# Optimization experiments

Hardware: AMD Instinct MI355X
Metric: run time of the kernel (lower is better)

The kernel has to match this reference:

```python
import jax, jax.numpy as jnp
import numpy as np

D_MODEL = 1024

def setup_inputs() -> dict:
    key = jax.random.key(0)
    k1, k2, k3, k4, k5 = jax.random.split(key, 5)
    B, T, C = 8, 4096, D_MODEL
    bound = 1.0 / np.sqrt(C)
    return {
        "x": jax.random.normal(k1, (B, T, C), dtype=jnp.float32),
        "W_state": jax.random.uniform(k2, (C, C), dtype=jnp.float32, minval=-bound, maxval=bound),
        "b_state": jax.random.uniform(k3, (C,), dtype=jnp.float32, minval=-bound, maxval=bound),
        "W_gate": jax.random.uniform(k4, (C, C), dtype=jnp.float32, minval=-bound, maxval=bound),
        "b_gate": jax.random.uniform(k5, (C,), dtype=jnp.float32, minval=-bound, maxval=bound),
    }

def reference(x, W_state, b_state, W_gate, b_gate):
    # x: [B, T, C]. Precompute both projections as large batched GEMMs
    # (input-dependent parts have no time dependency), then scan the
    # tanh recurrence + sigmoid gating over T.
    B, T, C = x.shape
    px = jnp.einsum('btc,dc->btd', x, W_state) + b_state          # [B,T,C]
    g = jax.nn.sigmoid(jnp.einsum('btc,dc->btd', x, W_gate) + b_gate)  # [B,T,C]

    def step(state, inp):
        p_t, g_t = inp                    # each [B, C]
        state = jnp.tanh(p_t + state)
        return state, g_t * state

    s0 = jnp.zeros((B, C), dtype=x.dtype)
    final_state, outs = jax.lax.scan(
        step, s0, (px.transpose(1, 0, 2), g.transpose(1, 0, 2)))
    return outs.transpose(1, 0, 2), final_state  # [B,T,C], [B,C]
```

## Files before the change

kernel.cpp:

```cpp
#include <hip/hip_runtime.h>

#define DB 8
#define DT 4096
#define DC 1024
#define GM (DB*DT)
#define GN (2*DC)
#define GK DC

#define SEG 128
#define NSEG (DT/SEG)
#define WU 64
#define UCH 16

typedef _Float16 f16;
typedef _Float16 f16x8 __attribute__((ext_vector_type(8)));
typedef _Float16 f16x4 __attribute__((ext_vector_type(4)));
typedef float    f32x4 __attribute__((ext_vector_type(4)));

__device__ __forceinline__ void async_copy16(const void* g, void* l) {
    __builtin_amdgcn_global_load_lds((const __attribute__((address_space(1))) void*)g,
                                     (__attribute__((address_space(3))) void*)l,
                                     16, 0, 0);
}

__global__ __launch_bounds__(256) void conv_x_kernel(const float* __restrict__ x,
                                                     f16* __restrict__ xh) {
    const size_t i = (size_t)blockIdx.x * 256 + threadIdx.x;
    const f32x4 v = *(const f32x4*)(x + 4*i);
    f16x4 h; h.x = (f16)v.x; h.y = (f16)v.y; h.z = (f16)v.z; h.w = (f16)v.w;
    *(f16x4*)(xh + 4*i) = h;
}

__global__ __launch_bounds__(256) void conv_w_kernel(const float* __restrict__ Ws,
                                                     const float* __restrict__ Wg,
                                                     f16* __restrict__ wc) {
    const int i = blockIdx.x * 256 + threadIdx.x;
    const int e = i * 4;
    const int n = e >> 10;
    const int k = e & 1023;
    const float* src = (n < DC) ? (Ws + (size_t)n * DC + k)
                                : (Wg + (size_t)(n - DC) * DC + k);
    const f32x4 v = *(const f32x4*)src;
    f16x4 h; h.x = (f16)v.x; h.y = (f16)v.y; h.z = (f16)v.z; h.w = (f16)v.w;
    *(f16x4*)(wc + e) = h;
}

template<bool GF16>
__global__ __launch_bounds__(256, 2) void gemm_kernel(
        const f16* __restrict__ xh, const f16* __restrict__ wc,
        const float* __restrict__ b_state, const float* __restrict__ b_gate,
        f16* __restrict__ pxh, f16* __restrict__ gh, float* __restrict__ outg) {
    __shared__ f16 lds_a[128 * 64];
    __shared__ f16 lds_b[128 * 64];

    const int tid  = threadIdx.x;
    const int lane = tid & 63;
    const int bn   = blockIdx.x & 15;
    const int bm   = blockIdx.x >> 4;
    const int wave = tid >> 6;
    const int wm   = (wave & 1) * 64;
    const int wn   = (wave >> 1) * 64;
    const int lr   = lane & 15;
    const int lq   = lane >> 4;

    f32x4 acc[4][4] = {};

    const int kc = tid & 7;
    const int rw = tid >> 3;
    const int ldsbase = (tid & 192) * 16;

    for (int kt = 0; kt < GK / 64; ++kt) {
        const int k0 = kt * 64;
        #pragma unroll
        for (int i = 0; i < 4; ++i) {
            const int row = i * 32 + rw;
            async_copy16(xh + (size_t)(bm * 128 + row) * GK + k0 + kc * 8,
                         (char*)lds_a + ldsbase + i * 4096);
            async_copy16(wc + (size_t)(bn * 128 + row) * GK + k0 + kc * 8,
                         (char*)lds_b + ldsbase + i * 4096);
        }
        __syncthreads();
        #pragma unroll
        for (int ks = 0; ks < 2; ++ks) {
            f16x8 af[4], bf[4];
            #pragma unroll
            for (int t = 0; t < 4; ++t) {
                af[t] = *(const f16x8*)&lds_a[(wm + t * 16 + lr) * 64 + ks * 32 + lq * 8];
                bf[t] = *(const f16x8*)&lds_b[(wn + t * 16 + lr) * 64 + ks * 32 + lq * 8];
            }
            #pragma unroll
            for (int im = 0; im < 4; ++im)
                #pragma unroll
                for (int in = 0; in < 4; ++in)
                    acc[im][in] = __builtin_amdgcn_mfma_f32_16x16x32_f16(
                        af[im], bf[in], acc[im][in], 0, 0, 0);
        }
        __syncthreads();
    }

    const int gm0 = bm * 128 + wm + lq * 4;
    const int gn0 = bn * 128 + wn + lr;
    if (bn < 8) {
        #pragma unroll
        for (int in = 0; in < 4; ++in) {
            const int gn = gn0 + in * 16;
            const float bias = b_state[gn];
            #pragma unroll
            for (int im = 0; im < 4; ++im) {
                const int gm = gm0 + im * 16;
                #pragma unroll
                for (int r = 0; r < 4; ++r)
                    pxh[(size_t)(gm + r) * DC + gn] = (f16)(acc[im][in][r] + bias);
            }
        }
    } else {
        #pragma unroll
        for (int in = 0; in < 4; ++in) {
            const int gn   = gn0 + in * 16;
            const int gcol = gn - DC;
            const float bias = b_gate[gcol];
            #pragma unroll
            for (int im = 0; im < 4; ++im) {
                const int gm = gm0 + im * 16;
                #pragma unroll
                for (int r = 0; r < 4; ++r) {
                    const float v = acc[im][in][r] + bias;
                    const float sg = 1.0f / (1.0f + __expf(-v));
                    if (GF16) gh[(size_t)(gm + r) * DC + gcol] = (f16)sg;
                    else      outg[(size_t)(gm + r) * DC + gcol] = sg;
                }
            }
        }
    }
}

template<bool GF16>
__global__ __launch_bounds__(256, 4) void scan_kernel(
        const f16* __restrict__ ph, const f16* __restrict__ gh,
        float* __restrict__ out) {
    const int tau   = blockIdx.x * 256 + threadIdx.x;
    const int seg   = tau >> 13;
    const int chain = tau & 8191;
    const size_t base = (size_t)(chain >> 10) * ((size_t)DT * DC) + (chain & 1023);
    const float L = 2.8853900817779268f;
    float sL = 0.0f, s = 0.0f;
    const int t0 = seg * SEG;

    if (seg) {
        const int tw = t0 - WU;
        f16 wA[UCH], wB[UCH];
        #pragma unroll
        for (int i = 0; i < UCH; ++i) wA[i] = ph[base + (size_t)(tw + i) * DC];
        #pragma unroll 1
        for (int ch = 0; ch < WU / UCH; ++ch) {
            #pragma unroll
            for (int i = 0; i < UCH; ++i)
                wB[i] = ph[base + (size_t)(tw + (ch + 1) * UCH + i) * DC];
            #pragma unroll
            for (int i = 0; i < UCH; ++i) {
                const float u = fmaf((float)wA[i], L, sL);
                const float e = __builtin_amdgcn_exp2f(u);
                const float r = __builtin_amdgcn_rcpf(e + 1.0f);
                sL = fmaf(-2.0f * L, r, L);
            }
            #pragma unroll
            for (int i = 0; i < UCH; ++i) wA[i] = wB[i];
        }
    }

    float pA[UCH], pB[UCH], gA[UCH], gB[UCH];
    #pragma unroll
    for (int i = 0; i < UCH; ++i) {
        const size_t idx = base + (size_t)(t0 + i) * DC;
        pA[i] = (float)ph[idx] * L;
        gA[i] = GF16 ? (float)gh[idx] : out[idx];
    }
    #pragma unroll 1
    for (int ch = 0; ch < SEG / UCH; ++ch) {
        if (GF16 || (ch + 1 < SEG / UCH)) {
            #pragma unroll
            for (int i = 0; i < UCH; ++i) {
                const size_t idx = base + (size_t)(t0 + (ch + 1) * UCH + i) * DC;
                pB[i] = (float)ph[idx] * L;
                gB[i] = GF16 ? (float)gh[idx] : out[idx];
            }
        }
        #pragma unroll
        for (int i = 0; i < UCH; ++i) {
            const float u = pA[i] + sL;
            const float e = __builtin_amdgcn_exp2f(u);
            const float r = __builtin_amdgcn_rcpf(e + 1.0f);
            s  = fmaf(-2.0f, r, 1.0f);
            sL = fmaf(-2.0f * L, r, L);
            out[base + (size_t)(t0 + ch * UCH + i) * DC] = gA[i] * s;
        }
        #pragma unroll
        for (int i = 0; i < UCH; ++i) { pA[i] = pB[i]; gA[i] = gB[i]; }
    }
    if (seg == NSEG - 1) out[(size_t)DB * DT * DC + chain] = s;
}

extern "C" void kernel_launch(void* const* d_in, const int* in_sizes, int n_in,
                              void* d_out, int out_size, void* d_ws, size_t ws_size,
                              hipStream_t stream) {
    const float* x  = (const float*)d_in[0];
    const float* Ws = (const float*)d_in[1];
    const float* bs = (const float*)d_in[2];
    const float* Wg = (const float*)d_in[3];
    const float* bg = (const float*)d_in[4];
    float* out = (float*)d_out;

    char* ws = (char*)d_ws;
    const size_t SZ_XH  = (size_t)GM * GK * 2;
    const size_t SZ_WC  = (size_t)GN * GK * 2;
    const size_t SZ_PXH = ((size_t)GM + UCH) * DC * 2;
    const size_t NEED_F16 = SZ_XH + SZ_WC + 2 * SZ_PXH;

    f16* xh = (f16*)ws;
    f16* wc = (f16*)(ws + SZ_XH);
    f16* pxh = (f16*)(ws + SZ_XH + SZ_WC);
    const bool gf16 = (ws_size >= NEED_F16);
    f16* gh = gf16 ? (f16*)(ws + SZ_XH + SZ_WC + SZ_PXH) : (f16*)nullptr;

    conv_x_kernel<<<dim3(GM * GK / 1024), dim3(256), 0, stream>>>(x, xh);
    conv_w_kernel<<<dim3(GN * GK / 1024), dim3(256), 0, stream>>>(Ws, Wg, wc);
    if (gf16) {
        gemm_kernel<true><<<dim3(4096), dim3(256), 0, stream>>>(
            xh, wc, bs, bg, pxh, gh, out);
        scan_kernel<true><<<dim3(1024), dim3(256), 0, stream>>>(pxh, gh, out);
    } else {
        gemm_kernel<false><<<dim3(4096), dim3(256), 0, stream>>>(
            xh, wc, bs, bg, pxh, gh, out);
        scan_kernel<false><<<dim3(1024), dim3(256), 0, stream>>>(pxh, gh, out);
    }
}
```

Baseline: 451.7 us.

## Swizzle GEMM LDS, remap blocks per XCD, shorten scan segments, drop fp32 gate path

The GEMM tile loads now use an XOR swizzle on the k-chunk index, so the MFMA fragment reads from LDS avoid bank conflicts. Block indices are remapped so each XCD works on a contiguous band of M rows, which should improve L2 reuse of the A tiles, and the occupancy hint rises to 4 blocks per CU. The scan segments are halved to 64 steps (with an 8-step chunk), doubling the parallel chains while keeping the same 64-step warm-up, so redundant warm-up work per output grows. The fallback that stored the fp32 gate in the output buffer is removed, so the code now assumes the workspace is large enough for the f16 gate buffer.

```diff
diff --git a/kernel.cpp b/kernel.cpp
--- a/kernel.cpp
+++ b/kernel.cpp
@@ -7,10 +7,10 @@
 #define GN (2*DC)
 #define GK DC
 
-#define SEG 128
+#define SEG 64
 #define NSEG (DT/SEG)
 #define WU 64
-#define UCH 16
+#define UCH 8
 
 typedef _Float16 f16;
 typedef _Float16 f16x8 __attribute__((ext_vector_type(8)));
@@ -45,18 +45,19 @@
     *(f16x4*)(wc + e) = h;
 }
 
-template<bool GF16>
-__global__ __launch_bounds__(256, 2) void gemm_kernel(
+__global__ __launch_bounds__(256, 4) void gemm_kernel(
         const f16* __restrict__ xh, const f16* __restrict__ wc,
         const float* __restrict__ b_state, const float* __restrict__ b_gate,
-        f16* __restrict__ pxh, f16* __restrict__ gh, float* __restrict__ outg) {
+        f16* __restrict__ pxh, f16* __restrict__ gh) {
     __shared__ f16 lds_a[128 * 64];
     __shared__ f16 lds_b[128 * 64];
 
     const int tid  = threadIdx.x;
     const int lane = tid & 63;
-    const int bn   = blockIdx.x & 15;
-    const int bm   = blockIdx.x >> 4;
+    const int xcd = blockIdx.x & 7;
+    const int lin = blockIdx.x >> 3;
+    const int bm  = xcd * 32 + (lin >> 4);
+    const int bn  = lin & 15;
     const int wave = tid >> 6;
     const int wm   = (wave & 1) * 64;
     const int wn   = (wave >> 1) * 64;
@@ -67,16 +68,18 @@
 
     const int kc = tid & 7;
     const int rw = tid >> 3;
+    const int kg = kc ^ (rw & 7);
     const int ldsbase = (tid & 192) * 16;
+    const int sw = lr & 7;
 
     for (int kt = 0; kt < GK / 64; ++kt) {
         const int k0 = kt * 64;
         #pragma unroll
         for (int i = 0; i < 4; ++i) {
             const int row = i * 32 + rw;
-            async_copy16(xh + (size_t)(bm * 128 + row) * GK + k0 + kc * 8,
+            async_copy16(xh + (size_t)(bm * 128 + row) * GK + k0 + kg * 8,
                          (char*)lds_a + ldsbase + i * 4096);
-            async_copy16(wc + (size_t)(bn * 128 + row) * GK + k0 + kc * 8,
+            async_copy16(wc + (size_t)(bn * 128 + row) * GK + k0 + kg * 8,
                          (char*)lds_b + ldsbase + i * 4096);
         }
         __syncthreads();
@@ -85,8 +88,9 @@
             f16x8 af[4], bf[4];
             #pragma unroll
             for (int t = 0; t < 4; ++t) {
-                af[t] = *(const f16x8*)&lds_a[(wm + t * 16 + lr) * 64 + ks * 32 + lq * 8];
-                bf[t] = *(const f16x8*)&lds_b[(wn + t * 16 + lr) * 64 + ks * 32 + lq * 8];
+                const int pc = (ks * 4 + lq) ^ sw;
+                af[t] = *(const f16x8*)&lds_a[(wm + t * 16 + lr) * 64 + pc * 8];
+                bf[t] = *(const f16x8*)&lds_b[(wn + t * 16 + lr) * 64 + pc * 8];
             }
             #pragma unroll
             for (int im = 0; im < 4; ++im)
@@ -125,16 +129,13 @@
                 #pragma unroll
                 for (int r = 0; r < 4; ++r) {
                     const float v = acc[im][in][r] + bias;
-                    const float sg = 1.0f / (1.0f + __expf(-v));
-                    if (GF16) gh[(size_t)(gm + r) * DC + gcol] = (f16)sg;
-                    else      outg[(size_t)(gm + r) * DC + gcol] = sg;
+                    gh[(size_t)(gm + r) * DC + gcol] = (f16)(1.0f / (1.0f + __expf(-v)));
                 }
             }
         }
     }
 }
 
-template<bool GF16>
 __global__ __launch_bounds__(256, 4) void scan_kernel(
         const f16* __restrict__ ph, const f16* __restrict__ gh,
         float* __restrict__ out) {
@@ -173,17 +174,15 @@
     for (int i = 0; i < UCH; ++i) {
         const size_t idx = base + (size_t)(t0 + i) * DC;
         pA[i] = (float)ph[idx] * L;
-        gA[i] = GF16 ? (float)gh[idx] : out[idx];
+        gA[i] = (float)gh[idx];
     }
     #pragma unroll 1
     for (int ch = 0; ch < SEG / UCH; ++ch) {
-        if (GF16 || (ch + 1 < SEG / UCH)) {
-            #pragma unroll
-            for (int i = 0; i < UCH; ++i) {
-                const size_t idx = base + (size_t)(t0 + (ch + 1) * UCH + i) * DC;
-                pB[i] = (float)ph[idx] * L;
-                gB[i] = GF16 ? (float)gh[idx] : out[idx];
-            }
+        #pragma unroll
+        for (int i = 0; i < UCH; ++i) {
+            const size_t idx = base + (size_t)(t0 + (ch + 1) * UCH + i) * DC;
+            pB[i] = (float)ph[idx] * L;
+            gB[i] = (float)gh[idx];
         }
         #pragma unroll
         for (int i = 0; i < UCH; ++i) {
@@ -213,24 +212,14 @@
     char* ws = (char*)d_ws;
     const size_t SZ_XH  = (size_t)GM * GK * 2;
     const size_t SZ_WC  = (size_t)GN * GK * 2;
-    const size_t SZ_PXH = ((size_t)GM + UCH) * DC * 2;
-    const size_t NEED_F16 = SZ_XH + SZ_WC + 2 * SZ_PXH;
-
-    f16* xh = (f16*)ws;
-    f16* wc = (f16*)(ws + SZ_XH);
+    const size_t SZ_PXH = ((size_t)GM + 16) * DC * 2;
+    f16* xh  = (f16*)ws;
+    f16* wc  = (f16*)(ws + SZ_XH);
     f16* pxh = (f16*)(ws + SZ_XH + SZ_WC);
-    const bool gf16 = (ws_size >= NEED_F16);
-    f16* gh = gf16 ? (f16*)(ws + SZ_XH + SZ_WC + SZ_PXH) : (f16*)nullptr;
+    f16* gh  = (f16*)(ws + SZ_XH + SZ_WC + SZ_PXH);
 
     conv_x_kernel<<<dim3(GM * GK / 1024), dim3(256), 0, stream>>>(x, xh);
     conv_w_kernel<<<dim3(GN * GK / 1024), dim3(256), 0, stream>>>(Ws, Wg, wc);
-    if (gf16) {
-        gemm_kernel<true><<<dim3(4096), dim3(256), 0, stream>>>(
-            xh, wc, bs, bg, pxh, gh, out);
-        scan_kernel<true><<<dim3(1024), dim3(256), 0, stream>>>(pxh, gh, out);
-    } else {
-        gemm_kernel<false><<<dim3(4096), dim3(256), 0, stream>>>(
-            xh, wc, bs, bg, pxh, gh, out);
-        scan_kernel<false><<<dim3(1024), dim3(256), 0, stream>>>(pxh, gh, out);
-    }
-}
+    gemm_kernel<<<dim3(4096), dim3(256), 0, stream>>>(xh, wc, bs, bg, pxh, gh);
+    scan_kernel<<<dim3(DB * DC * NSEG / 256), dim3(256), 0, stream>>>(pxh, gh, out);
+}
```

New measurement: 442.3 us. -2.1%, faster.
